# Optimization experiments

Hardware: AMD Instinct MI355X
Metric: run time of the kernel (lower is better)

Reference implementation:

```python
import jax, jax.numpy as jnp
import numpy as np

B, T, D, U = 64, 512, 512, 512


def setup_inputs() -> dict:
    key = jax.random.key(0)
    k1, k2, k3 = jax.random.split(key, 3)
    x = jax.random.normal(k1, (B, T, D), dtype=jnp.float32)
    Wk = jax.random.normal(k2, (D, 4 * U), dtype=jnp.float32) * (1.0 / np.sqrt(D))
    Wr = jax.random.normal(k3, (U, 4 * U), dtype=jnp.float32) * (1.0 / np.sqrt(U))
    # bias init per module: zeros(i), ones(f), zeros(g), zeros(o)
    b = jnp.concatenate([jnp.zeros(U), jnp.ones(U), jnp.zeros(2 * U)]).astype(jnp.float32)
    return {"x": x, "Wk": Wk, "Wr": Wr, "b": b}


def reference(x, Wk, Wr, b):
    units = Wr.shape[0]
    # Precompute input projection for all timesteps in one GEMM (same math).
    zx = jnp.einsum('btd,dk->btk', x, Wk)  # [B, T, 4U]
    h0 = jnp.zeros((x.shape[0], units), dtype=x.dtype)
    c0 = jnp.zeros((x.shape[0], units), dtype=x.dtype)

    def step(carry, zx_t):
        h, c = carry
        z = zx_t + h @ Wr + b  # [B, 4U]
        zi, zf, zg, zo = jnp.split(z, 4, axis=-1)
        i = jax.nn.sigmoid(zi)
        f = jax.nn.sigmoid(zf)
        c_new = f * c + i * jnp.tanh(zg)
        o = jax.nn.sigmoid(zo)
        h_new = o * jnp.tanh(c_new)
        return (h_new, c_new), None

    (h_last, c_last), _ = jax.lax.scan(step, (h0, c0), jnp.swapaxes(zx, 0, 1))
    # default flags: return_sequence=False, return_states=False -> last hidden
    return h_last
```

## Files before the change

### kernel.cpp

```cpp
#include <hip/hip_runtime.h>
#include <hip/hip_bf16.h>
#include <math.h>

#define BSZ 64
#define TT  512
#define DD  512
#define UU  512
#define NZ  2048

#define NSL    32
#define USL    16
#define NBG    4
#define BG     16
#define KSTEPS 16

using short8  = __attribute__((ext_vector_type(8))) short;
using floatx4 = __attribute__((ext_vector_type(4))) float;
typedef unsigned long long u64;

template <bool ZXBF16>
__global__ __launch_bounds__(256) void gemm_zx(const float* __restrict__ A,
                                               const float* __restrict__ B,
                                               void* __restrict__ Cout) {
  __shared__ float As[16][65];
  __shared__ float Bs[16][64];

  const int tid = threadIdx.x;
  const int tx = tid & 15;
  const int ty = tid >> 4;
  const int m0 = blockIdx.y * 64;
  const int n0 = blockIdx.x * 64;

  const int lm  = tid >> 2;
  const int lk4 = (tid & 3) * 4;
  const int lk  = tid >> 4;
  const int ln4 = (tid & 15) * 4;

  float acc[4][4] = {};

  for (int k0 = 0; k0 < DD; k0 += 16) {
    float4 av = *(const float4*)(A + (size_t)(m0 + lm) * DD + k0 + lk4);
    float4 bv = *(const float4*)(B + (size_t)(k0 + lk) * NZ + n0 + ln4);
    As[lk4 + 0][lm] = av.x;
    As[lk4 + 1][lm] = av.y;
    As[lk4 + 2][lm] = av.z;
    As[lk4 + 3][lm] = av.w;
    *(float4*)&Bs[lk][ln4] = bv;
    __syncthreads();
#pragma unroll
    for (int kk = 0; kk < 16; ++kk) {
      float a[4], b[4];
#pragma unroll
      for (int i = 0; i < 4; ++i) a[i] = As[kk][ty * 4 + i];
#pragma unroll
      for (int j = 0; j < 4; ++j) b[j] = Bs[kk][tx * 4 + j];
#pragma unroll
      for (int i = 0; i < 4; ++i)
#pragma unroll
        for (int j = 0; j < 4; ++j) acc[i][j] = fmaf(a[i], b[j], acc[i][j]);
    }
    __syncthreads();
  }

#pragma unroll
  for (int i = 0; i < 4; ++i) {
    const size_t row = (size_t)(m0 + ty * 4 + i) * NZ + n0 + tx * 4;
    if constexpr (ZXBF16) {
      __hip_bfloat16* C = (__hip_bfloat16*)Cout;
#pragma unroll
      for (int j = 0; j < 4; ++j) C[row + j] = __float2bfloat16(acc[i][j]);
    } else {
      float* C = (float*)Cout;
      *(float4*)&C[row] = make_float4(acc[i][0], acc[i][1], acc[i][2], acc[i][3]);
    }
  }
}

__device__ __forceinline__ floatx4 mfma16(short8 a, short8 b, floatx4 c) {
  return __builtin_amdgcn_mfma_f32_16x16x32_bf16(a, b, c, 0, 0, 0);
}

template <bool ZXBF16>
__global__ __launch_bounds__(256) void lstm_persist(
    const void* __restrict__ zx_, const float* __restrict__ Wr,
    const float* __restrict__ bias, unsigned short* __restrict__ h_hi,
    unsigned short* __restrict__ h_lo, int* __restrict__ flags,
    float* __restrict__ out) {
  extern __shared__ char lds[];
  unsigned short* wr_hi = (unsigned short*)lds;
  unsigned short* wr_lo = wr_hi + KSTEPS * 4 * 64 * 8;
  float* z_ex = (float*)(wr_lo + KSTEPS * 4 * 64 * 8);

  const int sl = blockIdx.x;
  const int bg = blockIdx.y;
  const int tid = threadIdx.x;
  const int g = tid >> 6;
  const int lane = tid & 63;
  const int u0 = sl * USL;

  {
    const int cidx = tid & 63;
    const int koff = tid >> 6;
    const int gg = cidx >> 4, u = cidx & 15;
    const int col = gg * UU + u0 + u;
    for (int k0 = 0; k0 < DD; k0 += 4) {
      const int k = k0 + koff;
      const float v = Wr[(size_t)k * NZ + col];
      const __hip_bfloat16 vh = __float2bfloat16(v);
      const float rem = v - __bfloat162float(vh);
      const __hip_bfloat16 vl = __float2bfloat16(rem);
      const int K = k >> 5, kg = (k >> 3) & 3, j = k & 7;
      const int off = ((K * 4 + gg) * 64 + (kg * 16 + u)) * 8 + j;
      wr_hi[off] = *(const unsigned short*)&vh;
      wr_lo[off] = *(const unsigned short*)&vl;
    }
  }
  __syncthreads();

  const int am = lane & 15, akg = lane >> 4;
  const size_t arow = (size_t)(bg * BG + am) * UU + akg * 8;

  const int eb = tid >> 4;
  const int eu = tid & 15;
  const int b = bg * BG + eb;
  const float bias_i = bias[0 * UU + u0 + eu];
  const float bias_f = bias[1 * UU + u0 + eu];
  const float bias_g = bias[2 * UU + u0 + eu];
  const float bias_o = bias[3 * UU + u0 + eu];
  float c_state = 0.f;
  const size_t plane_t = (size_t)BSZ * UU;
  const int wword = (b * UU + u0 + eu) >> 1;

  int* myflag = flags + (bg * NSL + sl) * 16;

  for (int t = 0; t < TT; ++t) {
    float zi, zf, zg, zo;
    {
      const size_t zb = ((size_t)b * TT + t) * NZ + u0 + eu;
      if constexpr (ZXBF16) {
        const unsigned short* zx = (const unsigned short*)zx_;
        zi = __bfloat162float(*(const __hip_bfloat16*)&zx[zb + 0 * UU]);
        zf = __bfloat162float(*(const __hip_bfloat16*)&zx[zb + 1 * UU]);
        zg = __bfloat162float(*(const __hip_bfloat16*)&zx[zb + 2 * UU]);
        zo = __bfloat162float(*(const __hip_bfloat16*)&zx[zb + 3 * UU]);
      } else {
        const float* zx = (const float*)zx_;
        zi = zx[zb + 0 * UU];
        zf = zx[zb + 1 * UU];
        zg = zx[zb + 2 * UU];
        zo = zx[zb + 3 * UU];
      }
    }

    if (tid < NSL) {
      const int* fp = flags + (bg * NSL + tid) * 16;
      while (__hip_atomic_load(fp, __ATOMIC_RELAXED, __HIP_MEMORY_SCOPE_AGENT) < t) {
      }
    }
    __syncthreads();
    __builtin_amdgcn_fence(__ATOMIC_ACQUIRE, "workgroup");

    const unsigned short* Ahi = h_hi + (size_t)t * plane_t + arow;
    const unsigned short* Alo = h_lo + (size_t)t * plane_t + arow;
    floatx4 a0 = {0, 0, 0, 0}, a1 = {0, 0, 0, 0}, a2 = {0, 0, 0, 0};
#pragma unroll 4
    for (int K = 0; K < KSTEPS; ++K) {
      const short8 ahi = *(const short8*)(Ahi + K * 32);
      const short8 alo = *(const short8*)(Alo + K * 32);
      const short8 bhi = *(const short8*)(wr_hi + ((K * 4 + g) * 64 + lane) * 8);
      const short8 blo = *(const short8*)(wr_lo + ((K * 4 + g) * 64 + lane) * 8);
      a0 = mfma16(ahi, bhi, a0);
      a1 = mfma16(ahi, blo, a1);
      a2 = mfma16(alo, bhi, a2);
    }
#pragma unroll
    for (int r = 0; r < 4; ++r) {
      const int bb = (lane >> 4) * 4 + r;
      z_ex[(g * 16 + bb) * 16 + (lane & 15)] = a0[r] + a1[r] + a2[r];
    }
    __syncthreads();

    zi += z_ex[(0 * 16 + eb) * 16 + eu] + bias_i;
    zf += z_ex[(1 * 16 + eb) * 16 + eu] + bias_f;
    zg += z_ex[(2 * 16 + eb) * 16 + eu] + bias_g;
    zo += z_ex[(3 * 16 + eb) * 16 + eu] + bias_o;

    const float ig = 1.f / (1.f + expf(-zi));
    const float fg = 1.f / (1.f + expf(-zf));
    const float gg = tanhf(zg);
    const float og = 1.f / (1.f + expf(-zo));
    c_state = fg * c_state + ig * gg;
    const float hn = og * tanhf(c_state);

    const __hip_bfloat16 hh = __float2bfloat16(hn);
    const float hrem = hn - __bfloat162float(hh);
    const __hip_bfloat16 hl = __float2bfloat16(hrem);
    const unsigned int vhi = (unsigned int)*(const unsigned short*)&hh;
    const unsigned int vlo = (unsigned int)*(const unsigned short*)&hl;
    const unsigned int phi_n = (unsigned int)__shfl_xor((int)vhi, 1);
    const unsigned int plo_n = (unsigned int)__shfl_xor((int)vlo, 1);
    if ((tid & 1) == 0) {
      const unsigned int whi = vhi | (phi_n << 16);
      const unsigned int wlo = vlo | (plo_n << 16);
      unsigned int* phi = (unsigned int*)(h_hi + (size_t)(t + 1) * plane_t) + wword;
      unsigned int* plo = (unsigned int*)(h_lo + (size_t)(t + 1) * plane_t) + wword;
      __hip_atomic_store(phi, whi, __ATOMIC_RELAXED, __HIP_MEMORY_SCOPE_AGENT);
      __hip_atomic_store(plo, wlo, __ATOMIC_RELAXED, __HIP_MEMORY_SCOPE_AGENT);
    }

    if (t == TT - 1) out[(size_t)b * UU + u0 + eu] = hn;

    __syncthreads();
    if (tid == 0)
      __hip_atomic_store(myflag, t + 1, __ATOMIC_RELAXED,
                         __HIP_MEMORY_SCOPE_AGENT);
  }
}

extern "C" void kernel_launch(void* const* d_in, const int* in_sizes, int n_in,
                              void* d_out, int out_size, void* d_ws, size_t ws_size,
                              hipStream_t stream) {
  const float* x    = (const float*)d_in[0];
  const float* Wk   = (const float*)d_in[1];
  const float* Wr   = (const float*)d_in[2];
  const float* bias = (const float*)d_in[3];
  float* out = (float*)d_out;

  const size_t plane_t = (size_t)BSZ * UU;
  const size_t hplane_bytes = (size_t)(TT + 1) * plane_t * 2;
  const size_t flags_bytes = (size_t)NBG * NSL * 16 * 4;
  const size_t zx_f32_bytes = (size_t)BSZ * TT * NZ * 4;

  const size_t need_f32 = zx_f32_bytes + 2 * hplane_bytes + flags_bytes;
  const bool use_bf16_zx = (ws_size < need_f32);
  const size_t zx_bytes = use_bf16_zx ? zx_f32_bytes / 2 : zx_f32_bytes;

  char* ws = (char*)d_ws;
  void* zx = (void*)ws;
  unsigned short* h_hi = (unsigned short*)(ws + zx_bytes);
  unsigned short* h_lo = (unsigned short*)(ws + zx_bytes + hplane_bytes);
  int* flags = (int*)(ws + zx_bytes + 2 * hplane_bytes);

  hipMemsetAsync(h_hi, 0, plane_t * 2, stream);
  hipMemsetAsync(h_lo, 0, plane_t * 2, stream);
  hipMemsetAsync(flags, 0, flags_bytes, stream);

  dim3 ggrid(NZ / 64, (BSZ * TT) / 64);
  if (use_bf16_zx)
    gemm_zx<true><<<ggrid, 256, 0, stream>>>(x, Wk, zx);
  else
    gemm_zx<false><<<ggrid, 256, 0, stream>>>(x, Wk, zx);

  const int lds_bytes = KSTEPS * 4 * 64 * 8 * 2 * 2 + 4 * 16 * 16 * 4;
  dim3 pgrid(NSL, NBG);
  if (use_bf16_zx) {
    hipFuncSetAttribute(reinterpret_cast<const void*>(lstm_persist<true>),
                        hipFuncAttributeMaxDynamicSharedMemorySize, lds_bytes);
    lstm_persist<true><<<pgrid, 256, lds_bytes, stream>>>(zx, Wr, bias, h_hi, h_lo,
                                                          flags, out);
  } else {
    hipFuncSetAttribute(reinterpret_cast<const void*>(lstm_persist<false>),
                        hipFuncAttributeMaxDynamicSharedMemorySize, lds_bytes);
    lstm_persist<false><<<pgrid, 256, lds_bytes, stream>>>(zx, Wr, bias, h_hi, h_lo,
                                                           flags, out);
  }
}
```

Baseline: 4.444 ms.

## Assign persistent LSTM blocks to batch groups by XCD for L2-local exchange

Launches 256 blocks and reads each block's XCC_ID, so every batch group is formed only from blocks running on the same XCD, with slots handed out by an atomic counter. The hidden-state exchange between the 32 slice blocks of a group then stays within one XCD's L2, which cuts cross-die coherence latency on each timestep. The h stores become plain stores instead of agent-scope atomic stores. This relies on each of XCDs 0-3 getting at least 32 resident blocks. If fewer arrive, groups never complete and the spin-wait deadlocks. It also relies on visibility ordering holding without the atomic stores.

After: 5.352 ms. 20.4% more time.

```diff
diff --git a/kernel.cpp b/kernel.cpp
--- a/kernel.cpp
+++ b/kernel.cpp
@@ -85,15 +85,29 @@
     const void* __restrict__ zx_, const float* __restrict__ Wr,
     const float* __restrict__ bias, unsigned short* __restrict__ h_hi,
     unsigned short* __restrict__ h_lo, int* __restrict__ flags,
-    float* __restrict__ out) {
+    int* __restrict__ xcd_ctr, float* __restrict__ out) {
+  __shared__ int s_role[2];
   extern __shared__ char lds[];
   unsigned short* wr_hi = (unsigned short*)lds;
   unsigned short* wr_lo = wr_hi + KSTEPS * 4 * 64 * 8;
   float* z_ex = (float*)(wr_lo + KSTEPS * 4 * 64 * 8);
 
-  const int sl = blockIdx.x;
-  const int bg = blockIdx.y;
   const int tid = threadIdx.x;
+
+  if (tid == 0) {
+    unsigned x;
+    asm volatile("s_getreg_b32 %0, hwreg(HW_REG_XCC_ID)" : "=s"(x));
+    const int xcd = (int)(x & 7u);
+    int slot = NSL;
+    if (xcd < NBG) slot = atomicAdd(&xcd_ctr[xcd * 16], 1);
+    s_role[0] = xcd;
+    s_role[1] = slot;
+  }
+  __syncthreads();
+  const int bg = s_role[0];
+  const int sl = s_role[1];
+  if (bg >= NBG || sl >= NSL) return;
+
   const int g = tid >> 6;
   const int lane = tid & 63;
   const int u0 = sl * USL;
@@ -204,8 +218,8 @@
       const unsigned int wlo = vlo | (plo_n << 16);
       unsigned int* phi = (unsigned int*)(h_hi + (size_t)(t + 1) * plane_t) + wword;
       unsigned int* plo = (unsigned int*)(h_lo + (size_t)(t + 1) * plane_t) + wword;
-      __hip_atomic_store(phi, whi, __ATOMIC_RELAXED, __HIP_MEMORY_SCOPE_AGENT);
-      __hip_atomic_store(plo, wlo, __ATOMIC_RELAXED, __HIP_MEMORY_SCOPE_AGENT);
+      *phi = whi;
+      *plo = wlo;
     }
 
     if (t == TT - 1) out[(size_t)b * UU + u0 + eu] = hn;
@@ -229,9 +243,10 @@
   const size_t plane_t = (size_t)BSZ * UU;
   const size_t hplane_bytes = (size_t)(TT + 1) * plane_t * 2;
   const size_t flags_bytes = (size_t)NBG * NSL * 16 * 4;
+  const size_t ctr_bytes = (size_t)8 * 16 * 4;
   const size_t zx_f32_bytes = (size_t)BSZ * TT * NZ * 4;
 
-  const size_t need_f32 = zx_f32_bytes + 2 * hplane_bytes + flags_bytes;
+  const size_t need_f32 = zx_f32_bytes + 2 * hplane_bytes + flags_bytes + ctr_bytes;
   const bool use_bf16_zx = (ws_size < need_f32);
   const size_t zx_bytes = use_bf16_zx ? zx_f32_bytes / 2 : zx_f32_bytes;
 
@@ -240,10 +255,11 @@
   unsigned short* h_hi = (unsigned short*)(ws + zx_bytes);
   unsigned short* h_lo = (unsigned short*)(ws + zx_bytes + hplane_bytes);
   int* flags = (int*)(ws + zx_bytes + 2 * hplane_bytes);
+  int* xcd_ctr = (int*)(ws + zx_bytes + 2 * hplane_bytes + flags_bytes);
 
   hipMemsetAsync(h_hi, 0, plane_t * 2, stream);
   hipMemsetAsync(h_lo, 0, plane_t * 2, stream);
-  hipMemsetAsync(flags, 0, flags_bytes, stream);
+  hipMemsetAsync(flags, 0, flags_bytes + ctr_bytes, stream);
 
   dim3 ggrid(NZ / 64, (BSZ * TT) / 64);
   if (use_bf16_zx)
@@ -252,16 +268,16 @@
     gemm_zx<false><<<ggrid, 256, 0, stream>>>(x, Wk, zx);
 
   const int lds_bytes = KSTEPS * 4 * 64 * 8 * 2 * 2 + 4 * 16 * 16 * 4;
-  dim3 pgrid(NSL, NBG);
+  dim3 pgrid(256);
   if (use_bf16_zx) {
     hipFuncSetAttribute(reinterpret_cast<const void*>(lstm_persist<true>),
                         hipFuncAttributeMaxDynamicSharedMemorySize, lds_bytes);
     lstm_persist<true><<<pgrid, 256, lds_bytes, stream>>>(zx, Wr, bias, h_hi, h_lo,
-                                                          flags, out);
+                                                          flags, xcd_ctr, out);
   } else {
     hipFuncSetAttribute(reinterpret_cast<const void*>(lstm_persist<false>),
                         hipFuncAttributeMaxDynamicSharedMemorySize, lds_bytes);
     lstm_persist<false><<<pgrid, 256, lds_bytes, stream>>>(zx, Wr, bias, h_hi, h_lo,
-                                                           flags, out);
-  }
-}
+                                                           flags, xcd_ctr, out);
+  }
+}
```

## Replace global barrier with per-chunk flag waits and interleaved h layout

Applied to the files above, without the earlier changes.

Replaces the per-step wait on all 32 slice flags followed by a workgroup barrier with per-wave waits on only the flag of the producer slice pair that owns each K chunk. The K loop is rotated per slice and its loads are software-pipelined 8 chunks ahead, so MFMA work can begin as soon as some chunks are ready. The hi/lo h planes are merged into one interleaved layout so each chunk is a single contiguous 128-byte block, and flags are padded to a larger stride. The next step's zx values are also prefetched during the current step. In exchange it adds more flag polling traffic and register pressure, and it relies on relaxed atomics plus a compiler barrier for ordering.

Result: slower. 4.704 ms (+5.8%).

```diff
diff --git a/kernel.cpp b/kernel.cpp
--- a/kernel.cpp
+++ b/kernel.cpp
@@ -13,6 +13,8 @@
 #define NBG    4
 #define BG     16
 #define KSTEPS 16
+#define FSTRIDE 32
+#define PF     8
 
 using short8  = __attribute__((ext_vector_type(8))) short;
 using floatx4 = __attribute__((ext_vector_type(4))) float;
@@ -83,9 +85,8 @@
 template <bool ZXBF16>
 __global__ __launch_bounds__(256) void lstm_persist(
     const void* __restrict__ zx_, const float* __restrict__ Wr,
-    const float* __restrict__ bias, unsigned short* __restrict__ h_hi,
-    unsigned short* __restrict__ h_lo, int* __restrict__ flags,
-    float* __restrict__ out) {
+    const float* __restrict__ bias, unsigned short* __restrict__ h_c,
+    int* __restrict__ flags, float* __restrict__ out) {
   extern __shared__ char lds[];
   unsigned short* wr_hi = (unsigned short*)lds;
   unsigned short* wr_lo = wr_hi + KSTEPS * 4 * 64 * 8;
@@ -97,6 +98,7 @@
   const int g = tid >> 6;
   const int lane = tid & 63;
   const int u0 = sl * USL;
+  const int K0 = sl >> 1;
 
   {
     const int cidx = tid & 63;
@@ -118,7 +120,8 @@
   __syncthreads();
 
   const int am = lane & 15, akg = lane >> 4;
-  const size_t arow = (size_t)(bg * BG + am) * UU + akg * 8;
+  const size_t arow_c = (size_t)(bg * BG + am) * (KSTEPS * 64) + akg * 8;
+  const size_t plane_c = (size_t)BSZ * KSTEPS * 64;
 
   const int eb = tid >> 4;
   const int eu = tid & 15;
@@ -128,51 +131,97 @@
   const float bias_g = bias[2 * UU + u0 + eu];
   const float bias_o = bias[3 * UU + u0 + eu];
   float c_state = 0.f;
-  const size_t plane_t = (size_t)BSZ * UU;
-  const int wword = (b * UU + u0 + eu) >> 1;
-
-  int* myflag = flags + (bg * NSL + sl) * 16;
+  const int mypair = sl >> 1;
+  const int wip = ((sl & 1) * 8) + (eu >> 1);
+
+  int* fbase = flags + bg * NSL * FSTRIDE;
+  int* myflag = fbase + sl * FSTRIDE;
+  const int fpar = lane & 1;
+  const size_t zbase = (size_t)b * TT;
+
+  float zi, zf, zg, zo;
+  {
+    const size_t zb = zbase * NZ + u0 + eu;
+    if constexpr (ZXBF16) {
+      const unsigned short* zx = (const unsigned short*)zx_;
+      zi = __bfloat162float(*(const __hip_bfloat16*)&zx[zb + 0 * UU]);
+      zf = __bfloat162float(*(const __hip_bfloat16*)&zx[zb + 1 * UU]);
+      zg = __bfloat162float(*(const __hip_bfloat16*)&zx[zb + 2 * UU]);
+      zo = __bfloat162float(*(const __hip_bfloat16*)&zx[zb + 3 * UU]);
+    } else {
+      const float* zx = (const float*)zx_;
+      zi = zx[zb + 0 * UU];
+      zf = zx[zb + 1 * UU];
+      zg = zx[zb + 2 * UU];
+      zo = zx[zb + 3 * UU];
+    }
+  }
 
   for (int t = 0; t < TT; ++t) {
-    float zi, zf, zg, zo;
-    {
-      const size_t zb = ((size_t)b * TT + t) * NZ + u0 + eu;
+    const unsigned short* Ab = h_c + (size_t)t * plane_c + arow_c;
+
+    int fv[KSTEPS];
+#pragma unroll
+    for (int j = 0; j < KSTEPS; ++j) {
+      const int K = (K0 + j) & 15;
+      fv[j] = __hip_atomic_load(fbase + (2 * K + fpar) * FSTRIDE,
+                                __ATOMIC_RELAXED, __HIP_MEMORY_SCOPE_AGENT);
+    }
+
+    short8 ah[PF], al[PF];
+#pragma unroll
+    for (int p = 0; p < PF; ++p) {
+      const int K = (K0 + p) & 15;
+      const int* fp = fbase + (2 * K + fpar) * FSTRIDE;
+      while (__any(fv[p] < t))
+        fv[p] = __hip_atomic_load(fp, __ATOMIC_RELAXED,
+                                  __HIP_MEMORY_SCOPE_AGENT);
+      asm volatile("" ::: "memory");
+      ah[p] = *(const short8*)(Ab + K * 64);
+      al[p] = *(const short8*)(Ab + K * 64 + 32);
+    }
+
+    float nzi = 0.f, nzf = 0.f, nzg = 0.f, nzo = 0.f;
+    if (t + 1 < TT) {
+      const size_t zb = (zbase + t + 1) * NZ + u0 + eu;
       if constexpr (ZXBF16) {
         const unsigned short* zx = (const unsigned short*)zx_;
-        zi = __bfloat162float(*(const __hip_bfloat16*)&zx[zb + 0 * UU]);
-        zf = __bfloat162float(*(const __hip_bfloat16*)&zx[zb + 1 * UU]);
-        zg = __bfloat162float(*(const __hip_bfloat16*)&zx[zb + 2 * UU]);
-        zo = __bfloat162float(*(const __hip_bfloat16*)&zx[zb + 3 * UU]);
+        nzi = __bfloat162float(*(const __hip_bfloat16*)&zx[zb + 0 * UU]);
+        nzf = __bfloat162float(*(const __hip_bfloat16*)&zx[zb + 1 * UU]);
+        nzg = __bfloat162float(*(const __hip_bfloat16*)&zx[zb + 2 * UU]);
+        nzo = __bfloat162float(*(const __hip_bfloat16*)&zx[zb + 3 * UU]);
       } else {
         const float* zx = (const float*)zx_;
-        zi = zx[zb + 0 * UU];
-        zf = zx[zb + 1 * UU];
-        zg = zx[zb + 2 * UU];
-        zo = zx[zb + 3 * UU];
+        nzi = zx[zb + 0 * UU];
+        nzf = zx[zb + 1 * UU];
+        nzg = zx[zb + 2 * UU];
+        nzo = zx[zb + 3 * UU];
       }
     }
 
-    if (tid < NSL) {
-      const int* fp = flags + (bg * NSL + tid) * 16;
-      while (__hip_atomic_load(fp, __ATOMIC_RELAXED, __HIP_MEMORY_SCOPE_AGENT) < t) {
+    floatx4 a0 = {0, 0, 0, 0}, a1 = {0, 0, 0, 0}, a2 = {0, 0, 0, 0};
+#pragma unroll
+    for (int j = 0; j < KSTEPS; ++j) {
+      const int K = (K0 + j) & 15;
+      const short8 Ah = ah[j & (PF - 1)];
+      const short8 Al = al[j & (PF - 1)];
+      if (j + PF < KSTEPS) {
+        const int Kp = (K0 + j + PF) & 15;
+        const int* fp = fbase + (2 * Kp + fpar) * FSTRIDE;
+        while (__any(fv[j + PF] < t))
+          fv[j + PF] = __hip_atomic_load(fp, __ATOMIC_RELAXED,
+                                         __HIP_MEMORY_SCOPE_AGENT);
+        asm volatile("" ::: "memory");
+        ah[j & (PF - 1)] = *(const short8*)(Ab + Kp * 64);
+        al[j & (PF - 1)] = *(const short8*)(Ab + Kp * 64 + 32);
       }
-    }
-    __syncthreads();
-    __builtin_amdgcn_fence(__ATOMIC_ACQUIRE, "workgroup");
-
-    const unsigned short* Ahi = h_hi + (size_t)t * plane_t + arow;
-    const unsigned short* Alo = h_lo + (size_t)t * plane_t + arow;
-    floatx4 a0 = {0, 0, 0, 0}, a1 = {0, 0, 0, 0}, a2 = {0, 0, 0, 0};
-#pragma unroll 4
-    for (int K = 0; K < KSTEPS; ++K) {
-      const short8 ahi = *(const short8*)(Ahi + K * 32);
-      const short8 alo = *(const short8*)(Alo + K * 32);
       const short8 bhi = *(const short8*)(wr_hi + ((K * 4 + g) * 64 + lane) * 8);
       const short8 blo = *(const short8*)(wr_lo + ((K * 4 + g) * 64 + lane) * 8);
-      a0 = mfma16(ahi, bhi, a0);
-      a1 = mfma16(ahi, blo, a1);
-      a2 = mfma16(alo, bhi, a2);
-    }
+      a0 = mfma16(Ah, bhi, a0);
+      a1 = mfma16(Ah, blo, a1);
+      a2 = mfma16(Al, bhi, a2);
+    }
+
 #pragma unroll
     for (int r = 0; r < 4; ++r) {
       const int bb = (lane >> 4) * 4 + r;
@@ -202,13 +251,17 @@
     if ((tid & 1) == 0) {
       const unsigned int whi = vhi | (phi_n << 16);
       const unsigned int wlo = vlo | (plo_n << 16);
-      unsigned int* phi = (unsigned int*)(h_hi + (size_t)(t + 1) * plane_t) + wword;
-      unsigned int* plo = (unsigned int*)(h_lo + (size_t)(t + 1) * plane_t) + wword;
-      __hip_atomic_store(phi, whi, __ATOMIC_RELAXED, __HIP_MEMORY_SCOPE_AGENT);
-      __hip_atomic_store(plo, wlo, __ATOMIC_RELAXED, __HIP_MEMORY_SCOPE_AGENT);
+      unsigned int* blk = (unsigned int*)h_c +
+                          (((size_t)(t + 1) * BSZ + b) * KSTEPS + mypair) * 32;
+      __hip_atomic_store(blk + wip, whi, __ATOMIC_RELAXED,
+                         __HIP_MEMORY_SCOPE_AGENT);
+      __hip_atomic_store(blk + 16 + wip, wlo, __ATOMIC_RELAXED,
+                         __HIP_MEMORY_SCOPE_AGENT);
     }
 
     if (t == TT - 1) out[(size_t)b * UU + u0 + eu] = hn;
+
+    zi = nzi; zf = nzf; zg = nzg; zo = nzo;
 
     __syncthreads();
     if (tid == 0)
@@ -226,23 +279,21 @@
   const float* bias = (const float*)d_in[3];
   float* out = (float*)d_out;
 
-  const size_t plane_t = (size_t)BSZ * UU;
-  const size_t hplane_bytes = (size_t)(TT + 1) * plane_t * 2;
-  const size_t flags_bytes = (size_t)NBG * NSL * 16 * 4;
+  const size_t plane_bytes = (size_t)BSZ * KSTEPS * 128;
+  const size_t h_bytes = (size_t)(TT + 1) * plane_bytes;
+  const size_t flags_bytes = (size_t)NBG * NSL * FSTRIDE * 4;
   const size_t zx_f32_bytes = (size_t)BSZ * TT * NZ * 4;
 
-  const size_t need_f32 = zx_f32_bytes + 2 * hplane_bytes + flags_bytes;
+  const size_t need_f32 = zx_f32_bytes + h_bytes + flags_bytes;
   const bool use_bf16_zx = (ws_size < need_f32);
   const size_t zx_bytes = use_bf16_zx ? zx_f32_bytes / 2 : zx_f32_bytes;
 
   char* ws = (char*)d_ws;
   void* zx = (void*)ws;
-  unsigned short* h_hi = (unsigned short*)(ws + zx_bytes);
-  unsigned short* h_lo = (unsigned short*)(ws + zx_bytes + hplane_bytes);
-  int* flags = (int*)(ws + zx_bytes + 2 * hplane_bytes);
-
-  hipMemsetAsync(h_hi, 0, plane_t * 2, stream);
-  hipMemsetAsync(h_lo, 0, plane_t * 2, stream);
+  unsigned short* h_c = (unsigned short*)(ws + zx_bytes);
+  int* flags = (int*)(ws + zx_bytes + h_bytes);
+
+  hipMemsetAsync(h_c, 0, plane_bytes, stream);
   hipMemsetAsync(flags, 0, flags_bytes, stream);
 
   dim3 ggrid(NZ / 64, (BSZ * TT) / 64);
@@ -256,12 +307,12 @@
   if (use_bf16_zx) {
     hipFuncSetAttribute(reinterpret_cast<const void*>(lstm_persist<true>),
                         hipFuncAttributeMaxDynamicSharedMemorySize, lds_bytes);
-    lstm_persist<true><<<pgrid, 256, lds_bytes, stream>>>(zx, Wr, bias, h_hi, h_lo,
+    lstm_persist<true><<<pgrid, 256, lds_bytes, stream>>>(zx, Wr, bias, h_c,
                                                           flags, out);
   } else {
     hipFuncSetAttribute(reinterpret_cast<const void*>(lstm_persist<false>),
                         hipFuncAttributeMaxDynamicSharedMemorySize, lds_bytes);
-    lstm_persist<false><<<pgrid, 256, lds_bytes, stream>>>(zx, Wr, bias, h_hi, h_lo,
+    lstm_persist<false><<<pgrid, 256, lds_bytes, stream>>>(zx, Wr, bias, h_c,
                                                            flags, out);
   }
 }
```

## Compute input projection with bf16 MFMA GEMM and always store zx in bf16

Applied to the files above, without the earlier changes.

Replaces the scalar fp32 tiled GEMM for the input projection with a bf16 MFMA GEMM. x and a transposed Wk are first converted to bf16 by small conversion kernels, staged in the h_hi/h_lo workspace regions before those are zeroed. The zx buffer is now always stored as bf16, which halves the write and read traffic for the recurrent kernel. In exchange the input projection loses precision because its inputs are rounded to bf16, not just its output, and two extra conversion passes are added.

New measurement: 3.671 ms. -17.4%, faster.

```diff
diff --git a/kernel.cpp b/kernel.cpp
--- a/kernel.cpp
+++ b/kernel.cpp
@@ -18,66 +18,80 @@
 using floatx4 = __attribute__((ext_vector_type(4))) float;
 typedef unsigned long long u64;
 
-template <bool ZXBF16>
-__global__ __launch_bounds__(256) void gemm_zx(const float* __restrict__ A,
-                                               const float* __restrict__ B,
-                                               void* __restrict__ Cout) {
-  __shared__ float As[16][65];
-  __shared__ float Bs[16][64];
-
-  const int tid = threadIdx.x;
-  const int tx = tid & 15;
-  const int ty = tid >> 4;
-  const int m0 = blockIdx.y * 64;
-  const int n0 = blockIdx.x * 64;
-
-  const int lm  = tid >> 2;
-  const int lk4 = (tid & 3) * 4;
-  const int lk  = tid >> 4;
-  const int ln4 = (tid & 15) * 4;
-
-  float acc[4][4] = {};
-
-  for (int k0 = 0; k0 < DD; k0 += 16) {
-    float4 av = *(const float4*)(A + (size_t)(m0 + lm) * DD + k0 + lk4);
-    float4 bv = *(const float4*)(B + (size_t)(k0 + lk) * NZ + n0 + ln4);
-    As[lk4 + 0][lm] = av.x;
-    As[lk4 + 1][lm] = av.y;
-    As[lk4 + 2][lm] = av.z;
-    As[lk4 + 3][lm] = av.w;
-    *(float4*)&Bs[lk][ln4] = bv;
-    __syncthreads();
-#pragma unroll
-    for (int kk = 0; kk < 16; ++kk) {
-      float a[4], b[4];
-#pragma unroll
-      for (int i = 0; i < 4; ++i) a[i] = As[kk][ty * 4 + i];
-#pragma unroll
-      for (int j = 0; j < 4; ++j) b[j] = Bs[kk][tx * 4 + j];
-#pragma unroll
-      for (int i = 0; i < 4; ++i)
-#pragma unroll
-        for (int j = 0; j < 4; ++j) acc[i][j] = fmaf(a[i], b[j], acc[i][j]);
-    }
-    __syncthreads();
-  }
-
-#pragma unroll
-  for (int i = 0; i < 4; ++i) {
-    const size_t row = (size_t)(m0 + ty * 4 + i) * NZ + n0 + tx * 4;
-    if constexpr (ZXBF16) {
-      __hip_bfloat16* C = (__hip_bfloat16*)Cout;
-#pragma unroll
-      for (int j = 0; j < 4; ++j) C[row + j] = __float2bfloat16(acc[i][j]);
-    } else {
-      float* C = (float*)Cout;
-      *(float4*)&C[row] = make_float4(acc[i][0], acc[i][1], acc[i][2], acc[i][3]);
-    }
-  }
-}
-
 __device__ __forceinline__ floatx4 mfma16(short8 a, short8 b, floatx4 c) {
   return __builtin_amdgcn_mfma_f32_16x16x32_bf16(a, b, c, 0, 0, 0);
+}
+
+__global__ __launch_bounds__(256) void conv_x(const float* __restrict__ x,
+                                              unsigned short* __restrict__ xb) {
+  const size_t base = ((size_t)blockIdx.x * 256 + threadIdx.x) * 8;
+  float4 a = *(const float4*)(x + base);
+  float4 b = *(const float4*)(x + base + 4);
+  short8 v;
+  const float va[8] = {a.x, a.y, a.z, a.w, b.x, b.y, b.z, b.w};
+#pragma unroll
+  for (int i = 0; i < 8; ++i) {
+    __hip_bfloat16 h = __float2bfloat16(va[i]);
+    v[i] = *(const short*)&h;
+  }
+  *(short8*)(xb + base) = v;
+}
+
+__global__ __launch_bounds__(256) void conv_wkt(const float* __restrict__ Wk,
+                                                unsigned short* __restrict__ wkt) {
+  const int n = blockIdx.x * 256 + threadIdx.x;
+  const int k0 = blockIdx.y * 8;
+  short8 v;
+#pragma unroll
+  for (int j = 0; j < 8; ++j) {
+    __hip_bfloat16 h = __float2bfloat16(Wk[(size_t)(k0 + j) * NZ + n]);
+    v[j] = *(const short*)&h;
+  }
+  *(short8*)(wkt + (size_t)n * DD + k0) = v;
+}
+
+__global__ __launch_bounds__(256) void gemm_zx_mfma(
+    const unsigned short* __restrict__ xb, const unsigned short* __restrict__ wkt,
+    __hip_bfloat16* __restrict__ C) {
+  __shared__ unsigned short As[64 * 40];
+  __shared__ unsigned short Bs[64 * 40];
+
+  const int tid = threadIdx.x;
+  const int w = tid >> 6;
+  const int lane = tid & 63;
+  const int n0 = blockIdx.x * 64;
+  const int m0 = blockIdx.y * 64;
+
+  const int srow = tid >> 2;
+  const int skq = tid & 3;
+
+  const int fm = (w * 16 + (lane & 15)) * 40 + (lane >> 4) * 8;
+  const int fu = (lane & 15) * 40 + (lane >> 4) * 8;
+
+  floatx4 acc[4] = {{0, 0, 0, 0}, {0, 0, 0, 0}, {0, 0, 0, 0}, {0, 0, 0, 0}};
+
+  for (int k0 = 0; k0 < DD; k0 += 32) {
+    const short8 av = *(const short8*)(xb + (size_t)(m0 + srow) * DD + k0 + skq * 8);
+    const short8 bv = *(const short8*)(wkt + (size_t)(n0 + srow) * DD + k0 + skq * 8);
+    *(short8*)&As[srow * 40 + skq * 8] = av;
+    *(short8*)&Bs[srow * 40 + skq * 8] = bv;
+    __syncthreads();
+    const short8 Af = *(const short8*)&As[fm];
+#pragma unroll
+    for (int ns = 0; ns < 4; ++ns) {
+      const short8 Bf = *(const short8*)&Bs[ns * 16 * 40 + fu];
+      acc[ns] = mfma16(Af, Bf, acc[ns]);
+    }
+    __syncthreads();
+  }
+
+  const int erow = m0 + w * 16 + (lane >> 4) * 4;
+  const int ecol = n0 + (lane & 15);
+#pragma unroll
+  for (int ns = 0; ns < 4; ++ns)
+#pragma unroll
+    for (int r = 0; r < 4; ++r)
+      C[(size_t)(erow + r) * NZ + ecol + ns * 16] = __float2bfloat16(acc[ns][r]);
 }
 
 template <bool ZXBF16>
@@ -229,39 +243,31 @@
   const size_t plane_t = (size_t)BSZ * UU;
   const size_t hplane_bytes = (size_t)(TT + 1) * plane_t * 2;
   const size_t flags_bytes = (size_t)NBG * NSL * 16 * 4;
-  const size_t zx_f32_bytes = (size_t)BSZ * TT * NZ * 4;
-
-  const size_t need_f32 = zx_f32_bytes + 2 * hplane_bytes + flags_bytes;
-  const bool use_bf16_zx = (ws_size < need_f32);
-  const size_t zx_bytes = use_bf16_zx ? zx_f32_bytes / 2 : zx_f32_bytes;
+  const size_t zx_bytes = (size_t)BSZ * TT * NZ * 2;
 
   char* ws = (char*)d_ws;
-  void* zx = (void*)ws;
+  __hip_bfloat16* zx = (__hip_bfloat16*)ws;
   unsigned short* h_hi = (unsigned short*)(ws + zx_bytes);
   unsigned short* h_lo = (unsigned short*)(ws + zx_bytes + hplane_bytes);
   int* flags = (int*)(ws + zx_bytes + 2 * hplane_bytes);
 
+  unsigned short* x_bf16 = h_hi;
+  unsigned short* wkt    = h_lo;
+
+  conv_x<<<dim3((BSZ * TT * DD) / (256 * 8)), 256, 0, stream>>>(x, x_bf16);
+  conv_wkt<<<dim3(NZ / 256, DD / 8), 256, 0, stream>>>(Wk, wkt);
+
+  gemm_zx_mfma<<<dim3(NZ / 64, (BSZ * TT) / 64), 256, 0, stream>>>(x_bf16, wkt,
+                                                                   zx);
+
   hipMemsetAsync(h_hi, 0, plane_t * 2, stream);
   hipMemsetAsync(h_lo, 0, plane_t * 2, stream);
   hipMemsetAsync(flags, 0, flags_bytes, stream);
 
-  dim3 ggrid(NZ / 64, (BSZ * TT) / 64);
-  if (use_bf16_zx)
-    gemm_zx<true><<<ggrid, 256, 0, stream>>>(x, Wk, zx);
-  else
-    gemm_zx<false><<<ggrid, 256, 0, stream>>>(x, Wk, zx);
-
   const int lds_bytes = KSTEPS * 4 * 64 * 8 * 2 * 2 + 4 * 16 * 16 * 4;
   dim3 pgrid(NSL, NBG);
-  if (use_bf16_zx) {
-    hipFuncSetAttribute(reinterpret_cast<const void*>(lstm_persist<true>),
-                        hipFuncAttributeMaxDynamicSharedMemorySize, lds_bytes);
-    lstm_persist<true><<<pgrid, 256, lds_bytes, stream>>>(zx, Wr, bias, h_hi, h_lo,
-                                                          flags, out);
-  } else {
-    hipFuncSetAttribute(reinterpret_cast<const void*>(lstm_persist<false>),
-                        hipFuncAttributeMaxDynamicSharedMemorySize, lds_bytes);
-    lstm_persist<false><<<pgrid, 256, lds_bytes, stream>>>(zx, Wr, bias, h_hi, h_lo,
-                                                           flags, out);
-  }
-}
+  hipFuncSetAttribute(reinterpret_cast<const void*>(lstm_persist<true>),
+                      hipFuncAttributeMaxDynamicSharedMemorySize, lds_bytes);
+  lstm_persist<true><<<pgrid, 256, lds_bytes, stream>>>(zx, Wr, bias, h_hi, h_lo,
+                                                        flags, out);
+}
```
